# Kernel optimization log

Hardware: AMD Instinct MI355X
Metric: run time of the kernel (lower is better)

## Reference

```python
import jax, jax.numpy as jnp
import numpy as np

N_NODES = 50000
N_EDGES = 300000
D = 256  # node/edge feature dim; MLP input = 3*D = 768


def setup_inputs() -> dict:
    key = jax.random.key(0)
    ks = jax.random.split(key, 5)
    x_node = jax.random.normal(ks[0], (N_NODES, D), dtype=jnp.float32)
    x_edge = jax.random.normal(ks[1], (N_EDGES, D), dtype=jnp.float32)
    edge_index = jax.random.randint(ks[2], (2, N_EDGES), 0, N_NODES, dtype=jnp.int64)
    # MLP params: Linear(3*D, D) -> ReLU -> Linear(D, D)
    W1 = jax.random.normal(ks[3], (3 * D, D), dtype=jnp.float32) * (1.0 / np.sqrt(3 * D))
    b1 = jnp.zeros((D,), dtype=jnp.float32)
    W2 = jax.random.normal(ks[4], (D, D), dtype=jnp.float32) * (1.0 / np.sqrt(D))
    b2 = jnp.zeros((D,), dtype=jnp.float32)
    return {"x_node": x_node, "x_edge": x_edge, "edge_index": edge_index,
            "W1": W1, "b1": b1, "W2": W2, "b2": b2}


def reference(x_node, x_edge, edge_index, W1, b1, W2, b2):
    # gather src/dst node feats and concat with edge feats: [E, 3*D]
    src = x_node[edge_index[0]]
    dst = x_node[edge_index[1]]
    h = jnp.concatenate([src, dst, x_edge], axis=1)
    # MLP (custom_func): Linear -> ReLU -> Linear
    h = jax.nn.relu(h @ W1 + b1)
    x_edge_ = h @ W2 + b2
    return x_edge_
```

## Files before the change

### kernel.cpp

```cpp
#include <hip/hip_runtime.h>
#include <hip/hip_bf16.h>


typedef __attribute__((ext_vector_type(8))) short short8;
typedef __attribute__((ext_vector_type(4))) float f32x4;

#define LDA 72
#define LDB 72
#define LDH 264

__device__ __forceinline__ unsigned short f2b(float f) {
  unsigned int u = __float_as_uint(f);
  unsigned int r = (u + 0x7FFFu + ((u >> 16) & 1u)) >> 16;
  return (unsigned short)r;
}

__global__ void transpose_w_kernel(const float* __restrict__ w,
                                   unsigned short* __restrict__ wt,
                                   int K, int N) {
  int i = blockIdx.x * 256 + threadIdx.x;
  if (i >= K * N) return;
  int n = i / K;
  int k = i - n * K;
  wt[i] = f2b(w[(size_t)k * N + n]);
}

__global__ void conv_bf16_kernel(const float* __restrict__ x,
                                 unsigned short* __restrict__ y, int n4) {
  int i = blockIdx.x * 256 + threadIdx.x;
  if (i >= n4) return;
  float4 v = ((const float4*)x)[i];
  ushort4 u;
  u.x = f2b(v.x); u.y = f2b(v.y); u.z = f2b(v.z); u.w = f2b(v.w);
  ((ushort4*)y)[i] = u;
}

__global__ __launch_bounds__(256, 2) void edge_mlp_kernel(
    const float* __restrict__ xnode, const float* __restrict__ xedge,
    const int* __restrict__ eidx,
    const unsigned short* __restrict__ nodeb, int use_nodeb,
    const unsigned short* __restrict__ wt1, const float* __restrict__ b1,
    const unsigned short* __restrict__ wt2, const float* __restrict__ b2,
    float* __restrict__ out, int E) {
  __shared__ __align__(16) unsigned short As[64 * LDA];
  __shared__ __align__(16) unsigned short Bs[256 * LDB];
  __shared__ __align__(16) unsigned short Hs[64 * LDH];

  const int t = threadIdx.x;
  const int w = t >> 6;
  const int l = t & 63;
  const int lr = l & 15;
  const int lk = l >> 4;

  const int ar = t >> 2;
  const int ac = t & 3;

  const int ebase = blockIdx.x * 64;
  int e = ebase + ar;
  if (e >= E) e = E - 1;
  const int isrc = eidx[e];
  const int idst = eidx[E + e];

  f32x4 acc[4][4];
#pragma unroll
  for (int i = 0; i < 4; ++i)
#pragma unroll
    for (int j = 0; j < 4; ++j) acc[i][j] = (f32x4)0.0f;

  for (int kc = 0; kc < 12; ++kc) {
    const int seg = kc >> 2;
    const int kin = (kc & 3) * 64;

    if (use_nodeb && seg < 2) {
      const int row = (seg == 0) ? isrc : idst;
      const unsigned short* sp = nodeb + (size_t)row * 256 + kin + ac * 16;
      uint4 v0 = *(const uint4*)(sp);
      uint4 v1 = *(const uint4*)(sp + 8);
      *(uint4*)&As[ar * LDA + ac * 16] = v0;
      *(uint4*)&As[ar * LDA + ac * 16 + 8] = v1;
    } else {
      const float* sp =
          ((seg == 0) ? xnode + (size_t)isrc * 256
                      : (seg == 1) ? xnode + (size_t)idst * 256
                                   : xedge + (size_t)e * 256) + kin + ac * 16;
#pragma unroll
      for (int q = 0; q < 4; ++q) {
        float4 v = *(const float4*)(sp + q * 4);
        ushort4 u;
        u.x = f2b(v.x); u.y = f2b(v.y); u.z = f2b(v.z); u.w = f2b(v.w);
        *(ushort4*)&As[ar * LDA + ac * 16 + q * 4] = u;
      }
    }

    {
      const unsigned short* wp = wt1 + kc * 64 + (t & 7) * 8;
      const int n0 = t >> 3;
#pragma unroll
      for (int i = 0; i < 8; ++i) {
        const int n = n0 + 32 * i;
        uint4 v = *(const uint4*)(wp + (size_t)n * 768);
        *(uint4*)&Bs[n * LDB + (t & 7) * 8] = v;
      }
    }
    __syncthreads();

#pragma unroll
    for (int ks = 0; ks < 2; ++ks) {
      short8 af[4], bf[4];
#pragma unroll
      for (int mi = 0; mi < 4; ++mi)
        af[mi] = *(const short8*)&As[(mi * 16 + lr) * LDA + ks * 32 + lk * 8];
#pragma unroll
      for (int ni = 0; ni < 4; ++ni)
        bf[ni] = *(const short8*)&Bs[(w * 64 + ni * 16 + lr) * LDB + ks * 32 + lk * 8];
#pragma unroll
      for (int mi = 0; mi < 4; ++mi)
#pragma unroll
        for (int ni = 0; ni < 4; ++ni)
          acc[mi][ni] = __builtin_amdgcn_mfma_f32_16x16x32_bf16(
              af[mi], bf[ni], acc[mi][ni], 0, 0, 0);
    }
    __syncthreads();
  }

#pragma unroll
  for (int ni = 0; ni < 4; ++ni) {
    const int col = w * 64 + ni * 16 + lr;
    const float bias = b1[col];
#pragma unroll
    for (int mi = 0; mi < 4; ++mi) {
#pragma unroll
      for (int r = 0; r < 4; ++r) {
        float v = acc[mi][ni][r] + bias;
        v = v > 0.f ? v : 0.f;
        Hs[(mi * 16 + lk * 4 + r) * LDH + col] = f2b(v);
        acc[mi][ni][r] = 0.f;
      }
    }
  }
  __syncthreads();

  for (int kc = 0; kc < 4; ++kc) {
    {
      const unsigned short* wp = wt2 + kc * 64 + (t & 7) * 8;
      const int n0 = t >> 3;
#pragma unroll
      for (int i = 0; i < 8; ++i) {
        const int n = n0 + 32 * i;
        uint4 v = *(const uint4*)(wp + (size_t)n * 256);
        *(uint4*)&Bs[n * LDB + (t & 7) * 8] = v;
      }
    }
    __syncthreads();

#pragma unroll
    for (int ks = 0; ks < 2; ++ks) {
      short8 af[4], bf[4];
#pragma unroll
      for (int mi = 0; mi < 4; ++mi)
        af[mi] = *(const short8*)&Hs[(mi * 16 + lr) * LDH + kc * 64 + ks * 32 + lk * 8];
#pragma unroll
      for (int ni = 0; ni < 4; ++ni)
        bf[ni] = *(const short8*)&Bs[(w * 64 + ni * 16 + lr) * LDB + ks * 32 + lk * 8];
#pragma unroll
      for (int mi = 0; mi < 4; ++mi)
#pragma unroll
        for (int ni = 0; ni < 4; ++ni)
          acc[mi][ni] = __builtin_amdgcn_mfma_f32_16x16x32_bf16(
              af[mi], bf[ni], acc[mi][ni], 0, 0, 0);
    }
    __syncthreads();
  }

#pragma unroll
  for (int ni = 0; ni < 4; ++ni) {
    const int col = w * 64 + ni * 16 + lr;
    const float bias = b2[col];
#pragma unroll
    for (int mi = 0; mi < 4; ++mi) {
#pragma unroll
      for (int r = 0; r < 4; ++r) {
        const int ee = ebase + mi * 16 + lk * 4 + r;
        if (ee < E) out[(size_t)ee * 256 + col] = acc[mi][ni][r] + bias;
      }
    }
  }
}

extern "C" void kernel_launch(void* const* d_in, const int* in_sizes, int n_in,
                              void* d_out, int out_size, void* d_ws, size_t ws_size,
                              hipStream_t stream) {
  const float* xnode = (const float*)d_in[0];
  const float* xedge = (const float*)d_in[1];
  const int* eidx = (const int*)d_in[2];
  const float* W1 = (const float*)d_in[3];
  const float* b1 = (const float*)d_in[4];
  const float* W2 = (const float*)d_in[5];
  const float* b2 = (const float*)d_in[6];
  float* out = (float*)d_out;

  const int NN = in_sizes[0] / 256;
  const int E = in_sizes[1] / 256;

  char* ws = (char*)d_ws;
  unsigned short* wt1 = (unsigned short*)ws;
  unsigned short* wt2 = (unsigned short*)(ws + 768 * 256 * 2);
  unsigned short* nodeb = (unsigned short*)(ws + 768 * 256 * 2 + 256 * 256 * 2);
  const size_t need = (size_t)768 * 256 * 2 + 256 * 256 * 2 + (size_t)NN * 256 * 2;
  const int use_nodeb = (ws_size >= need) ? 1 : 0;

  transpose_w_kernel<<<(768 * 256 + 255) / 256, 256, 0, stream>>>(W1, wt1, 768, 256);
  transpose_w_kernel<<<(256 * 256 + 255) / 256, 256, 0, stream>>>(W2, wt2, 256, 256);
  if (use_nodeb) {
    const int n4 = NN * 64;
    conv_bf16_kernel<<<(n4 + 255) / 256, 256, 0, stream>>>(xnode, nodeb, n4);
  }

  edge_mlp_kernel<<<(E + 63) / 64, 256, 0, stream>>>(
      xnode, xedge, eidx, nodeb, use_nodeb, wt1, b1, wt2, b2, out, E);
}
```

Before: 390.7 us.

## Double-buffer edge MLP with direct global-to-LDS loads and 128-edge tiles

Reworks the fused edge MLP kernel. Tiles grow to 128 edges with 512 threads, and A/B tiles are double-buffered so the next K-chunk is loaded while the current one runs on MFMA. Weights are prepacked into per-chunk tiles and streamed with global_load_lds, the hidden layer in LDS uses an XOR swizzle, and output is staged through LDS for coalesced float4 stores. The cost is 112KB of shared memory per block, which limits occupancy.

```diff
diff --git a/kernel.cpp b/kernel.cpp
--- a/kernel.cpp
+++ b/kernel.cpp
@@ -1,28 +1,38 @@
 #include <hip/hip_runtime.h>
-#include <hip/hip_bf16.h>
 
 
 typedef __attribute__((ext_vector_type(8))) short short8;
 typedef __attribute__((ext_vector_type(4))) float f32x4;
 
-#define LDA 72
-#define LDB 72
-#define LDH 264
+typedef __attribute__((address_space(1))) unsigned int* gp1_t;
+typedef __attribute__((address_space(3))) unsigned int* lp3_t;
+
+#define AS_OFF 0
+#define BS_OFF 16384
+#define HS_OFF 49152
+#define SMEM_SZ 114688
+#define LDO 260
 
 __device__ __forceinline__ unsigned short f2b(float f) {
   unsigned int u = __float_as_uint(f);
-  unsigned int r = (u + 0x7FFFu + ((u >> 16) & 1u)) >> 16;
-  return (unsigned short)r;
-}
-
-__global__ void transpose_w_kernel(const float* __restrict__ w,
-                                   unsigned short* __restrict__ wt,
-                                   int K, int N) {
+  return (unsigned short)((u + 0x7FFFu + ((u >> 16) & 1u)) >> 16);
+}
+__device__ __forceinline__ unsigned int f2b2(float lo, float hi) {
+  return (unsigned int)f2b(lo) | ((unsigned int)f2b(hi) << 16);
+}
+__device__ __forceinline__ void gload16(const void* g, void* l) {
+  __builtin_amdgcn_global_load_lds((gp1_t)g, (lp3_t)l, 16, 0, 0);
+}
+
+__global__ void prep_w_kernel(const float* __restrict__ w,
+                              unsigned short* __restrict__ wp, int total) {
   int i = blockIdx.x * 256 + threadIdx.x;
-  if (i >= K * N) return;
-  int n = i / K;
-  int k = i - n * K;
-  wt[i] = f2b(w[(size_t)k * N + n]);
+  if (i >= total) return;
+  int kc = i >> 13;
+  int rem = i & 8191;
+  int n = rem >> 5;
+  int kin = rem & 31;
+  wp[i] = f2b(w[(size_t)(kc * 32 + kin) * 256 + n]);
 }
 
 __global__ void conv_bf16_kernel(const float* __restrict__ x,
@@ -35,31 +45,29 @@
   ((ushort4*)y)[i] = u;
 }
 
-__global__ __launch_bounds__(256, 2) void edge_mlp_kernel(
+__global__ __launch_bounds__(512, 2) void edge_mlp_kernel(
     const float* __restrict__ xnode, const float* __restrict__ xedge,
     const int* __restrict__ eidx,
     const unsigned short* __restrict__ nodeb, int use_nodeb,
-    const unsigned short* __restrict__ wt1, const float* __restrict__ b1,
-    const unsigned short* __restrict__ wt2, const float* __restrict__ b2,
+    const unsigned short* __restrict__ wt1p, const float* __restrict__ b1,
+    const unsigned short* __restrict__ wt2p, const float* __restrict__ b2,
     float* __restrict__ out, int E) {
-  __shared__ __align__(16) unsigned short As[64 * LDA];
-  __shared__ __align__(16) unsigned short Bs[256 * LDB];
-  __shared__ __align__(16) unsigned short Hs[64 * LDH];
+  __shared__ __align__(16) char smem[SMEM_SZ];
+  char* As = smem + AS_OFF;
+  char* Bs = smem + BS_OFF;
+  char* Hs = smem + HS_OFF;
 
   const int t = threadIdx.x;
-  const int w = t >> 6;
-  const int l = t & 63;
-  const int lr = l & 15;
-  const int lk = l >> 4;
-
-  const int ar = t >> 2;
-  const int ac = t & 3;
-
-  const int ebase = blockIdx.x * 64;
-  int e = ebase + ar;
+  const int w = t >> 6, l = t & 63;
+  const int lr = l & 15, lk = l >> 4;
+  const int wr = w >> 2, wc = w & 3;
+  const int row4 = t >> 2;
+  const int c4 = t & 3;
+
+  const int ebase = blockIdx.x * 128;
+  int e = ebase + row4;
   if (e >= E) e = E - 1;
-  const int isrc = eidx[e];
-  const int idst = eidx[E + e];
+  const int isrc = eidx[e], idst = eidx[E + e];
 
   f32x4 acc[4][4];
 #pragma unroll
@@ -67,52 +75,114 @@
 #pragma unroll
     for (int j = 0; j < 4; ++j) acc[i][j] = (f32x4)0.0f;
 
-  for (int kc = 0; kc < 12; ++kc) {
-    const int seg = kc >> 2;
-    const int kin = (kc & 3) * 64;
-
-    if (use_nodeb && seg < 2) {
-      const int row = (seg == 0) ? isrc : idst;
-      const unsigned short* sp = nodeb + (size_t)row * 256 + kin + ac * 16;
-      uint4 v0 = *(const uint4*)(sp);
-      uint4 v1 = *(const uint4*)(sp + 8);
-      *(uint4*)&As[ar * LDA + ac * 16] = v0;
-      *(uint4*)&As[ar * LDA + ac * 16 + 8] = v1;
+  auto stageB = [&](const unsigned short* wp, int kc, int buf) {
+    const char* g = (const char*)wp + (size_t)kc * 16384 + t * 16;
+    char* lb = Bs + buf * 16384 + (w << 10);
+    gload16(g, lb);
+    gload16(g + 8192, lb + 8192);
+  };
+  auto stageA_node = [&](int kc, int buf) {
+    const int node = (kc < 8) ? isrc : idst;
+    const char* g = (const char*)nodeb + (size_t)node * 512 + (kc & 7) * 64 + c4 * 16;
+    gload16(g, As + buf * 8192 + (w << 10));
+  };
+  auto stageA_load = [&](int kc, float4& m0, float4& m1) {
+    const float* src;
+    if (kc < 8)        src = xnode + (size_t)isrc * 256 + kc * 32 + c4 * 8;
+    else if (kc < 16)  src = xnode + (size_t)idst * 256 + (kc - 8) * 32 + c4 * 8;
+    else               src = xedge + (size_t)e * 256 + (kc - 16) * 32 + c4 * 8;
+    m0 = *(const float4*)src;
+    m1 = *(const float4*)(src + 4);
+  };
+  auto stageA_write = [&](int buf, float4 m0, float4 m1) {
+    uint4 u;
+    u.x = f2b2(m0.x, m0.y); u.y = f2b2(m0.z, m0.w);
+    u.z = f2b2(m1.x, m1.y); u.w = f2b2(m1.z, m1.w);
+    *(uint4*)(As + buf * 8192 + t * 16) = u;
+  };
+
+  auto compute1 = [&](int buf) {
+    short8 af[4], bf[4];
+    const char* ab = As + buf * 8192;
+    const char* bb = Bs + buf * 16384;
+#pragma unroll
+    for (int mi = 0; mi < 4; ++mi)
+      af[mi] = *(const short8*)(ab + (wr * 64 + mi * 16 + lr) * 64 + lk * 16);
+#pragma unroll
+    for (int ni = 0; ni < 4; ++ni)
+      bf[ni] = *(const short8*)(bb + (wc * 64 + ni * 16 + lr) * 64 + lk * 16);
+#pragma unroll
+    for (int mi = 0; mi < 4; ++mi)
+#pragma unroll
+      for (int ni = 0; ni < 4; ++ni)
+        acc[mi][ni] = __builtin_amdgcn_mfma_f32_16x16x32_bf16(
+            af[mi], bf[ni], acc[mi][ni], 0, 0, 0);
+  };
+
+  stageB(wt1p, 0, 0);
+  if (use_nodeb) {
+    stageA_node(0, 0);
+  } else {
+    float4 a0, a1;
+    stageA_load(0, a0, a1);
+    stageA_write(0, a0, a1);
+  }
+  __syncthreads();
+
+  for (int kc = 0; kc < 24; ++kc) {
+    const int cur = kc & 1, nb = cur ^ 1;
+    float4 m0, m1;
+    bool man = false;
+    if (kc < 23) {
+      const int nk = kc + 1;
+      stageB(wt1p, nk, nb);
+      if (use_nodeb && nk < 16) {
+        stageA_node(nk, nb);
+      } else {
+        stageA_load(nk, m0, m1);
+        man = true;
+      }
     } else {
-      const float* sp =
-          ((seg == 0) ? xnode + (size_t)isrc * 256
-                      : (seg == 1) ? xnode + (size_t)idst * 256
-                                   : xedge + (size_t)e * 256) + kin + ac * 16;
-#pragma unroll
-      for (int q = 0; q < 4; ++q) {
-        float4 v = *(const float4*)(sp + q * 4);
-        ushort4 u;
-        u.x = f2b(v.x); u.y = f2b(v.y); u.z = f2b(v.z); u.w = f2b(v.w);
-        *(ushort4*)&As[ar * LDA + ac * 16 + q * 4] = u;
-      }
-    }
-
+      stageB(wt2p, 0, nb);
+    }
+    compute1(cur);
+    if (man) stageA_write(nb, m0, m1);
+    __syncthreads();
+  }
+
+#pragma unroll
+  for (int ni = 0; ni < 4; ++ni) {
+    const int col = wc * 64 + ni * 16 + lr;
+    const float bias = b1[col];
+    const int chunk = col >> 3;
+    const int cb = (col & 7) * 2;
+#pragma unroll
+    for (int mi = 0; mi < 4; ++mi)
+#pragma unroll
+      for (int r = 0; r < 4; ++r) {
+        const int row = wr * 64 + mi * 16 + lk * 4 + r;
+        float v = acc[mi][ni][r] + bias;
+        v = v > 0.f ? v : 0.f;
+        *(unsigned short*)(Hs + row * 512 + ((chunk ^ (row & 7)) * 16) + cb) = f2b(v);
+        acc[mi][ni][r] = 0.f;
+      }
+  }
+  __syncthreads();
+
+  for (int kc2 = 0; kc2 < 8; ++kc2) {
+    const int cur = kc2 & 1, nb = cur ^ 1;
+    if (kc2 < 7) stageB(wt2p, kc2 + 1, nb);
     {
-      const unsigned short* wp = wt1 + kc * 64 + (t & 7) * 8;
-      const int n0 = t >> 3;
-#pragma unroll
-      for (int i = 0; i < 8; ++i) {
-        const int n = n0 + 32 * i;
-        uint4 v = *(const uint4*)(wp + (size_t)n * 768);
-        *(uint4*)&Bs[n * LDB + (t & 7) * 8] = v;
-      }
-    }
-    __syncthreads();
-
-#pragma unroll
-    for (int ks = 0; ks < 2; ++ks) {
       short8 af[4], bf[4];
-#pragma unroll
-      for (int mi = 0; mi < 4; ++mi)
-        af[mi] = *(const short8*)&As[(mi * 16 + lr) * LDA + ks * 32 + lk * 8];
+      const char* bb = Bs + cur * 16384;
+#pragma unroll
+      for (int mi = 0; mi < 4; ++mi) {
+        const int row = wr * 64 + mi * 16 + lr;
+        af[mi] = *(const short8*)(Hs + row * 512 + (((kc2 * 4 + lk) ^ (row & 7)) * 16));
+      }
 #pragma unroll
       for (int ni = 0; ni < 4; ++ni)
-        bf[ni] = *(const short8*)&Bs[(w * 64 + ni * 16 + lr) * LDB + ks * 32 + lk * 8];
+        bf[ni] = *(const short8*)(bb + (wc * 64 + ni * 16 + lr) * 64 + lk * 16);
 #pragma unroll
       for (int mi = 0; mi < 4; ++mi)
 #pragma unroll
@@ -123,66 +193,32 @@
     __syncthreads();
   }
 
-#pragma unroll
-  for (int ni = 0; ni < 4; ++ni) {
-    const int col = w * 64 + ni * 16 + lr;
-    const float bias = b1[col];
-#pragma unroll
-    for (int mi = 0; mi < 4; ++mi) {
-#pragma unroll
-      for (int r = 0; r < 4; ++r) {
-        float v = acc[mi][ni][r] + bias;
-        v = v > 0.f ? v : 0.f;
-        Hs[(mi * 16 + lk * 4 + r) * LDH + col] = f2b(v);
-        acc[mi][ni][r] = 0.f;
-      }
-    }
-  }
-  __syncthreads();
-
-  for (int kc = 0; kc < 4; ++kc) {
-    {
-      const unsigned short* wp = wt2 + kc * 64 + (t & 7) * 8;
-      const int n0 = t >> 3;
-#pragma unroll
-      for (int i = 0; i < 8; ++i) {
-        const int n = n0 + 32 * i;
-        uint4 v = *(const uint4*)(wp + (size_t)n * 256);
-        *(uint4*)&Bs[n * LDB + (t & 7) * 8] = v;
-      }
-    }
-    __syncthreads();
-
-#pragma unroll
-    for (int ks = 0; ks < 2; ++ks) {
-      short8 af[4], bf[4];
-#pragma unroll
-      for (int mi = 0; mi < 4; ++mi)
-        af[mi] = *(const short8*)&Hs[(mi * 16 + lr) * LDH + kc * 64 + ks * 32 + lk * 8];
-#pragma unroll
-      for (int ni = 0; ni < 4; ++ni)
-        bf[ni] = *(const short8*)&Bs[(w * 64 + ni * 16 + lr) * LDB + ks * 32 + lk * 8];
-#pragma unroll
-      for (int mi = 0; mi < 4; ++mi)
-#pragma unroll
-        for (int ni = 0; ni < 4; ++ni)
-          acc[mi][ni] = __builtin_amdgcn_mfma_f32_16x16x32_bf16(
-              af[mi], bf[ni], acc[mi][ni], 0, 0, 0);
-    }
-    __syncthreads();
-  }
-
-#pragma unroll
-  for (int ni = 0; ni < 4; ++ni) {
-    const int col = w * 64 + ni * 16 + lr;
-    const float bias = b2[col];
-#pragma unroll
-    for (int mi = 0; mi < 4; ++mi) {
-#pragma unroll
-      for (int r = 0; r < 4; ++r) {
-        const int ee = ebase + mi * 16 + lk * 4 + r;
-        if (ee < E) out[(size_t)ee * 256 + col] = acc[mi][ni][r] + bias;
-      }
+  float* outst = (float*)smem;
+#pragma unroll
+  for (int p = 0; p < 2; ++p) {
+    __syncthreads();
+    if (wr == p) {
+#pragma unroll
+      for (int ni = 0; ni < 4; ++ni) {
+        const int col = wc * 64 + ni * 16 + lr;
+        const float bias = b2[col];
+#pragma unroll
+        for (int mi = 0; mi < 4; ++mi)
+#pragma unroll
+          for (int r = 0; r < 4; ++r)
+            outst[(mi * 16 + lk * 4 + r) * LDO + col] = acc[mi][ni][r] + bias;
+      }
+    }
+    __syncthreads();
+#pragma unroll
+    for (int it = 0; it < 8; ++it) {
+      const int idx = it * 2048 + t * 4;
+      const int lrow = idx >> 8;
+      const int cc = idx & 255;
+      const int grow = ebase + p * 64 + lrow;
+      if (grow < E)
+        *(float4*)(out + (size_t)grow * 256 + cc) =
+            *(const float4*)(outst + lrow * LDO + cc);
     }
   }
 }
@@ -203,19 +239,19 @@
   const int E = in_sizes[1] / 256;
 
   char* ws = (char*)d_ws;
-  unsigned short* wt1 = (unsigned short*)ws;
-  unsigned short* wt2 = (unsigned short*)(ws + 768 * 256 * 2);
-  unsigned short* nodeb = (unsigned short*)(ws + 768 * 256 * 2 + 256 * 256 * 2);
-  const size_t need = (size_t)768 * 256 * 2 + 256 * 256 * 2 + (size_t)NN * 256 * 2;
+  unsigned short* wt1p = (unsigned short*)ws;
+  unsigned short* wt2p = (unsigned short*)(ws + 24 * 16384);
+  unsigned short* nodeb = (unsigned short*)(ws + 32 * 16384);
+  const size_t need = (size_t)32 * 16384 + (size_t)NN * 512;
   const int use_nodeb = (ws_size >= need) ? 1 : 0;
 
-  transpose_w_kernel<<<(768 * 256 + 255) / 256, 256, 0, stream>>>(W1, wt1, 768, 256);
-  transpose_w_kernel<<<(256 * 256 + 255) / 256, 256, 0, stream>>>(W2, wt2, 256, 256);
+  prep_w_kernel<<<(24 * 8192 + 255) / 256, 256, 0, stream>>>(W1, wt1p, 24 * 8192);
+  prep_w_kernel<<<(8 * 8192 + 255) / 256, 256, 0, stream>>>(W2, wt2p, 8 * 8192);
   if (use_nodeb) {
     const int n4 = NN * 64;
     conv_bf16_kernel<<<(n4 + 255) / 256, 256, 0, stream>>>(xnode, nodeb, n4);
   }
 
-  edge_mlp_kernel<<<(E + 63) / 64, 256, 0, stream>>>(
-      xnode, xedge, eidx, nodeb, use_nodeb, wt1, b1, wt2, b2, out, E);
-}
+  edge_mlp_kernel<<<(E + 127) / 128, 512, 0, stream>>>(
+      xnode, xedge, eidx, nodeb, use_nodeb, wt1p, b1, wt2p, b2, out, E);
+}
```

Result: faster. 332.2 us (-15.0%).
